# Kernel tuning notes

Measured on AMD Instinct MI355X. Metric: run time of the kernel, lower is better.

## Reference

```python
import jax, jax.numpy as jnp
import numpy as np

N, C, O, H, S, SHARE = 30000, 128, 128, 8, 16, 8
D = O // H            # mid_planes = 16
OS = O // SHARE       # 16
OFFSETS = [15000, 30000]
EPS = 1e-5


def _knn(p, offsets, k):
    """Exact per-batch KNN (incl. self), chunked to bound memory."""
    n = p.shape[0]
    idx = np.empty((n, k), dtype=np.int64)
    start = 0
    for end in offsets:
        pb = p[start:end]
        sq = (pb * pb).sum(-1)
        for qs in range(0, pb.shape[0], 1024):
            q = pb[qs:qs + 1024]
            d = sq[qs:qs + q.shape[0], None] - 2.0 * (q @ pb.T) + sq[None, :]
            part = np.argpartition(d, k - 1, axis=1)[:, :k]
            idx[start + qs:start + qs + q.shape[0]] = part + start
        start = end
    return idx


def _ln(x, g, b):
    m = x.mean(-1, keepdims=True)
    v = ((x - m) ** 2).mean(-1, keepdims=True)
    return (x - m) / jnp.sqrt(v + EPS) * g + b


def setup_inputs() -> dict:
    rng = np.random.default_rng(0)
    p_np = (rng.standard_normal((N, 3)) * 5.0).astype(np.float32)
    idx = _knn(p_np, OFFSETS, S)

    key = jax.random.key(0)
    ks = jax.random.split(key, 12)

    def lin(k, i, o):
        return (jax.random.normal(k, (i, o), jnp.float32) / np.sqrt(i)).astype(jnp.float32)

    return {
        "p": jnp.asarray(p_np),
        "x": jax.random.normal(ks[0], (N, C), jnp.float32),
        "idx": jnp.asarray(idx),
        "Wq": lin(ks[1], C, O), "bq": jnp.zeros((O,), jnp.float32),
        "Wk": lin(ks[2], C, O), "bk": jnp.zeros((O,), jnp.float32),
        "Wv": lin(ks[3], C, O), "bv": jnp.zeros((O,), jnp.float32),
        "Wp1": lin(ks[4], 3, 3), "bp1": jnp.zeros((3,), jnp.float32),
        "gp": jnp.ones((3,), jnp.float32), "betap": jnp.zeros((3,), jnp.float32),
        "Wp2": lin(ks[5], 3, O), "bp2": jnp.zeros((O,), jnp.float32),
        "gw1": jnp.ones((D,), jnp.float32), "betaw1": jnp.zeros((D,), jnp.float32),
        "Ww1": lin(ks[6], D, OS), "bw1": jnp.zeros((OS,), jnp.float32),
        "gw2": jnp.ones((OS,), jnp.float32), "betaw2": jnp.zeros((OS,), jnp.float32),
        "Ww2": lin(ks[7], OS, OS), "bw2": jnp.zeros((OS,), jnp.float32),
    }


def reference(p, x, idx, Wq, bq, Wk, bk, Wv, bv, Wp1, bp1, gp, betap, Wp2, bp2,
              gw1, betaw1, Ww1, bw1, gw2, betaw2, Ww2, bw2):
    xq = (x @ Wq + bq).reshape(N, H, D)          # (N,H,D)
    xk = x @ Wk + bk                              # (N,O)
    xv = x @ Wv + bv
    kg = xk[idx].reshape(N, S, H, D)              # neighbor gather
    vg = xv[idx].reshape(N, S, H, D)
    pr = p[idx] - p[:, None, :]                   # relative coords (N,S,3)
    pe = jax.nn.relu(_ln(pr @ Wp1 + bp1, gp, betap)) @ Wp2 + bp2  # (N,S,O)
    pe = pe.reshape(N, S, H, D)
    r = kg + pe - xq[:, None]                     # (N,S,H,D)
    w = jax.nn.relu(_ln(r, gw1, betaw1)) @ Ww1 + bw1
    w = jax.nn.relu(_ln(w, gw2, betaw2)) @ Ww2 + bw2  # (N,S,H,OS)
    w = jax.nn.softmax(w.mean(-1), axis=1)        # softmax over the S neighbors
    out = ((vg + pe) * w[..., None]).sum(axis=1)  # weighted neighbor reduce
    return out.reshape(N, O)
```

## Files before the change

### kernel.cpp

```cpp
#include <hip/hip_runtime.h>
#include <math.h>

typedef unsigned int  uint;
typedef unsigned short ushort;

constexpr int NPTS = 30000;
constexpr int CIN  = 128;
constexpr int OC   = 128;
constexpr int NH   = 8;
constexpr int NS   = 16;
constexpr int DH   = 16;
constexpr int OSH  = 16;
constexpr float EPSF = 1e-5f;

typedef __attribute__((ext_vector_type(8))) __fp16 h8;
typedef __attribute__((ext_vector_type(4))) float  f32x4;
typedef __attribute__((ext_vector_type(2))) __fp16 h2;

__device__ __forceinline__ ushort f2h(float f) {
    __fp16 h = (__fp16)f;
    return *(ushort*)&h;
}
__device__ __forceinline__ uint pk2(float a, float b) {
    h2 v = __builtin_amdgcn_cvt_pkrtz(a, b);
    return *(uint*)&v;
}
__device__ __forceinline__ h2 asH2(uint u) { return *(h2*)&u; }

#if defined(__has_builtin)
#if __has_builtin(__builtin_elementwise_max)
#define PKMAX(a, b) __builtin_elementwise_max(a, b)
#endif
#endif
#ifndef PKMAX
__device__ __forceinline__ h2 PKMAX(h2 a, h2 b) {
    h2 r; r[0] = a[0] > b[0] ? a[0] : b[0]; r[1] = a[1] > b[1] ? a[1] : b[1]; return r;
}
#endif

constexpr int PK_WW1   = 0;
constexpr int PK_WP2   = 128;
constexpr int PK_BP2   = 320;
constexpr int PK_GW1   = 384;
constexpr int PK_BW1P  = 392;
constexpr int PK_GW2   = 400;
constexpr int PK_BW2P  = 408;
constexpr int PK_RM    = 416;
constexpr int PKF_BW1  = 424;
constexpr int PKF_RMB  = 440;

__global__ __launch_bounds__(256) void prep_kernel(
    const float* __restrict__ Wq, const float* __restrict__ Wk, const float* __restrict__ Wv,
    const float* __restrict__ Wp2, const float* __restrict__ bp2,
    const float* __restrict__ gw1, const float* __restrict__ betaw1,
    const float* __restrict__ Ww1, const float* __restrict__ bw1,
    const float* __restrict__ gw2, const float* __restrict__ betaw2,
    const float* __restrict__ Ww2, const float* __restrict__ bw2,
    ushort* __restrict__ WT, uint* __restrict__ PK)
{
    const int b = blockIdx.x;
    const int t = threadIdx.x;
    if (b < 24) {
        const int mat = b >> 3;
        const int cg  = b & 7;
        const float* W = (mat == 0) ? Wq : (mat == 1 ? Wk : Wv);
        const int col = cg * 16 + (t >> 4);
        const int k0  = (t & 15) * 8;
        float v0 = W[(k0 + 0) * OC + col], v1 = W[(k0 + 1) * OC + col];
        float v2 = W[(k0 + 2) * OC + col], v3 = W[(k0 + 3) * OC + col];
        float v4 = W[(k0 + 4) * OC + col], v5 = W[(k0 + 5) * OC + col];
        float v6 = W[(k0 + 6) * OC + col], v7 = W[(k0 + 7) * OC + col];
        uint4 u = make_uint4(pk2(v0, v1), pk2(v2, v3), pk2(v4, v5), pk2(v6, v7));
        *(uint4*)&WT[(size_t)mat * OC * CIN + (size_t)col * CIN + k0] = u;
    } else {
        float* FPK = (float*)PK;
        if (t < 128) {
            int dp = t >> 4, o = t & 15;
            PK[PK_WW1 + t] = pk2(Ww1[(2 * dp) * OSH + o], Ww1[(2 * dp + 1) * OSH + o]);
        }
        if (t < 192) {
            int c = t >> 6, jj = t & 63;
            PK[PK_WP2 + t] = pk2(Wp2[c * OC + 2 * jj], Wp2[c * OC + 2 * jj + 1]);
        }
        if (t < 64)
            PK[PK_BP2 + t] = pk2(bp2[2 * t], bp2[2 * t + 1]);
        if (t < 8) {
            PK[PK_GW1 + t]  = pk2(gw1[2 * t],    gw1[2 * t + 1]);
            PK[PK_BW1P + t] = pk2(betaw1[2 * t], betaw1[2 * t + 1]);
            PK[PK_GW2 + t]  = pk2(gw2[2 * t],    gw2[2 * t + 1]);
            PK[PK_BW2P + t] = pk2(betaw2[2 * t], betaw2[2 * t + 1]);
            float r0 = 0.f, r1 = 0.f;
            #pragma unroll
            for (int o2 = 0; o2 < OSH; ++o2) {
                r0 += Ww2[(2 * t) * OSH + o2];
                r1 += Ww2[(2 * t + 1) * OSH + o2];
            }
            PK[PK_RM + t] = pk2(r0 * (1.f / OSH), r1 * (1.f / OSH));
        }
        if (t < 16)
            FPK[PKF_BW1 + t] = bw1[t];
        if (t == 16) {
            float acc = 0.f;
            #pragma unroll
            for (int o2 = 0; o2 < OSH; ++o2) acc += bw2[o2];
            FPK[PKF_RMB] = acc * (1.f / OSH);
        }
    }
}

__global__ __launch_bounds__(256) void qkv_mfma(
    const float* __restrict__ x, const ushort* __restrict__ WT,
    const float* __restrict__ bq, const float* __restrict__ bk, const float* __restrict__ bv,
    ushort* __restrict__ yq, ushort* __restrict__ yk, ushort* __restrict__ yv)
{
    const int mat = blockIdx.y;
    const float* bias = (mat == 0) ? bq : (mat == 1 ? bk : bv);
    ushort* y         = (mat == 0) ? yq : (mat == 1 ? yk : yv);
    const ushort* T   = WT + (size_t)mat * OC * CIN;

    const int n0   = blockIdx.x * 128;
    const int t    = threadIdx.x;
    const int wave = t >> 6;
    const int lane = t & 63;
    const int m16  = lane & 15;
    const int quad = lane >> 4;

    f32x4 acc[2][8];
    #pragma unroll
    for (int mt = 0; mt < 2; ++mt)
        #pragma unroll
        for (int nt = 0; nt < 8; ++nt)
            acc[mt][nt] = (f32x4){0.f, 0.f, 0.f, 0.f};

    int r0i = n0 + wave * 32 + m16;
    int r1i = r0i + 16;
    if (r0i > NPTS - 1) r0i = NPTS - 1;
    if (r1i > NPTS - 1) r1i = NPTS - 1;
    const float* arow0 = x + (size_t)r0i * CIN;
    const float* arow1 = x + (size_t)r1i * CIN;

    #pragma unroll
    for (int ks = 0; ks < 4; ++ks) {
        const int kb = ks * 32 + quad * 8;
        float4 f00 = *(const float4*)(arow0 + kb);
        float4 f01 = *(const float4*)(arow0 + kb + 4);
        float4 f10 = *(const float4*)(arow1 + kb);
        float4 f11 = *(const float4*)(arow1 + kb + 4);
        uint4 ua0 = make_uint4(pk2(f00.x, f00.y), pk2(f00.z, f00.w),
                               pk2(f01.x, f01.y), pk2(f01.z, f01.w));
        uint4 ua1 = make_uint4(pk2(f10.x, f10.y), pk2(f10.z, f10.w),
                               pk2(f11.x, f11.y), pk2(f11.z, f11.w));
        h8 a0 = *(h8*)&ua0;
        h8 a1 = *(h8*)&ua1;
        #pragma unroll
        for (int nt = 0; nt < 8; ++nt) {
            h8 bfr = *(const h8*)(T + (size_t)(nt * 16 + m16) * CIN + kb);
            acc[0][nt] = __builtin_amdgcn_mfma_f32_16x16x32_f16(a0, bfr, acc[0][nt], 0, 0, 0);
            acc[1][nt] = __builtin_amdgcn_mfma_f32_16x16x32_f16(a1, bfr, acc[1][nt], 0, 0, 0);
        }
    }

    #pragma unroll
    for (int mt = 0; mt < 2; ++mt) {
        #pragma unroll
        for (int nt = 0; nt < 8; ++nt) {
            const int col = nt * 16 + m16;
            const float bcol = bias[col];
            #pragma unroll
            for (int r = 0; r < 4; ++r) {
                int row = n0 + wave * 32 + mt * 16 + quad * 4 + r;
                if (row < NPTS)
                    y[(size_t)row * OC + col] = f2h(acc[mt][nt][r] + bcol);
            }
        }
    }
}

__global__ __launch_bounds__(256) void attn_kernel(
    const float* __restrict__ p, const int* __restrict__ idx,
    const ushort* __restrict__ xq, const ushort* __restrict__ xk, const ushort* __restrict__ xv,
    const float* __restrict__ Wp1, const float* __restrict__ bp1,
    const float* __restrict__ gp,  const float* __restrict__ betap,
    const uint* __restrict__ PK,
    float* __restrict__ out)
{
    const int t    = threadIdx.x;
    const int wv   = t >> 6;
    const int lane = t & 63;
    const int n    = blockIdx.x * 4 + wv;
    const int s    = lane & 15;
    const int u    = lane >> 4;

    const float* FPK = (const float*)PK;

    __shared__ __attribute__((aligned(16))) char pool[4 * 16 * 272];
    char* red = pool + wv * (16 * 272);

    const int j = idx[n * NS + s];

    float t0, t1, t2;
    {
        float pr0 = p[j * 3 + 0] - p[n * 3 + 0];
        float pr1 = p[j * 3 + 1] - p[n * 3 + 1];
        float pr2 = p[j * 3 + 2] - p[n * 3 + 2];
        float uu[3];
        #pragma unroll
        for (int c = 0; c < 3; ++c)
            uu[c] = bp1[c] + pr0 * Wp1[0 * 3 + c] + pr1 * Wp1[1 * 3 + c] + pr2 * Wp1[2 * 3 + c];
        float m   = (uu[0] + uu[1] + uu[2]) * (1.f / 3.f);
        float d0 = uu[0] - m, d1 = uu[1] - m, d2 = uu[2] - m;
        float var = (d0 * d0 + d1 * d1 + d2 * d2) * (1.f / 3.f);
        float inv = rsqrtf(var + EPSF);
        t0 = fmaxf((uu[0] - m) * inv * gp[0] + betap[0], 0.f);
        t1 = fmaxf((uu[1] - m) * inv * gp[1] + betap[1], 0.f);
        t2 = fmaxf((uu[2] - m) * inv * gp[2] + betap[2], 0.f);
    }

    __attribute__((aligned(16))) h2 pe2[16];
    {
        h2 t02 = asH2(pk2(t0, t0));
        h2 t12 = asH2(pk2(t1, t1));
        h2 t22 = asH2(pk2(t2, t2));
        const uint* W0p = PK + PK_WP2 + 0 * 64 + u * 16;
        const uint* W1p = PK + PK_WP2 + 1 * 64 + u * 16;
        const uint* W2p = PK + PK_WP2 + 2 * 64 + u * 16;
        const uint* Bp  = PK + PK_BP2 + u * 16;
        #pragma unroll
        for (int i = 0; i < 16; ++i) {
            h2 acc = asH2(Bp[i]);
            acc = acc + t02 * asH2(W0p[i]);
            acc = acc + t12 * asH2(W1p[i]);
            acc = acc + t22 * asH2(W2p[i]);
            pe2[i] = acc;
        }
    }

    __attribute__((aligned(16))) h2 vp2[16], r2[16];
    {
        __attribute__((aligned(16))) h2 k2[16], q2[16], v2[16];
        const uint4* k4 = (const uint4*)(xk + (size_t)j * OC + u * 32);
        const uint4* v4 = (const uint4*)(xv + (size_t)j * OC + u * 32);
        const uint4* q4 = (const uint4*)(xq + (size_t)n * OC + u * 32);
        #pragma unroll
        for (int i = 0; i < 4; ++i) {
            *(uint4*)&k2[4 * i] = k4[i];
            *(uint4*)&v2[4 * i] = v4[i];
            *(uint4*)&q2[4 * i] = q4[i];
        }
        #pragma unroll
        for (int i = 0; i < 16; ++i) {
            r2[i]  = (k2[i] + pe2[i]) - q2[i];
            vp2[i] = v2[i] + pe2[i];
        }
    }

    float wgt[2];
    #pragma unroll
    for (int hh = 0; hh < 2; ++hh) {
        h2* rr = r2 + hh * 8;

        __attribute__((aligned(16))) h2 a2[8];
        {
            h2 sum2 = rr[0];
            #pragma unroll
            for (int i = 1; i < 8; ++i) sum2 = sum2 + rr[i];
            float m = ((float)sum2[0] + (float)sum2[1]) * (1.f / DH);
            h2 m2 = asH2(pk2(m, m));
            h2 vs2 = {(__fp16)0.f, (__fp16)0.f};
            #pragma unroll
            for (int i = 0; i < 8; ++i) {
                rr[i] = rr[i] - m2;
                vs2 = vs2 + rr[i] * rr[i];
            }
            float var = ((float)vs2[0] + (float)vs2[1]) * (1.f / DH);
            float inv = rsqrtf(var + EPSF);
            h2 inv2 = asH2(pk2(inv, inv));
            h2 z2 = {(__fp16)0.f, (__fp16)0.f};
            #pragma unroll
            for (int i = 0; i < 8; ++i) {
                h2 gi = asH2(PK[PK_GW1 + i]) * inv2;
                a2[i] = PKMAX(rr[i] * gi + asH2(PK[PK_BW1P + i]), z2);
            }
        }

        float w1[OSH];
        #pragma unroll
        for (int o2 = 0; o2 < OSH; ++o2) w1[o2] = FPK[PKF_BW1 + o2];
        #pragma unroll
        for (int dp = 0; dp < 8; ++dp) {
            #pragma unroll
            for (int o2 = 0; o2 < OSH; ++o2)
                w1[o2] = __builtin_amdgcn_fdot2(a2[dp], asH2(PK[PK_WW1 + dp * 16 + o2]), w1[o2], false);
        }

        float logit;
        {
            __attribute__((aligned(16))) h2 w2[8];
            #pragma unroll
            for (int i = 0; i < 8; ++i) w2[i] = asH2(pk2(w1[2 * i], w1[2 * i + 1]));
            h2 sum2 = w2[0];
            #pragma unroll
            for (int i = 1; i < 8; ++i) sum2 = sum2 + w2[i];
            float m = ((float)sum2[0] + (float)sum2[1]) * (1.f / OSH);
            h2 m2 = asH2(pk2(m, m));
            h2 vs2 = {(__fp16)0.f, (__fp16)0.f};
            #pragma unroll
            for (int i = 0; i < 8; ++i) {
                w2[i] = w2[i] - m2;
                vs2 = vs2 + w2[i] * w2[i];
            }
            float var = ((float)vs2[0] + (float)vs2[1]) * (1.f / OSH);
            float inv = rsqrtf(var + EPSF);
            h2 inv2 = asH2(pk2(inv, inv));
            h2 z2 = {(__fp16)0.f, (__fp16)0.f};
            logit = FPK[PKF_RMB];
            #pragma unroll
            for (int i = 0; i < 8; ++i) {
                h2 gi = asH2(PK[PK_GW2 + i]) * inv2;
                h2 bv2 = PKMAX(w2[i] * gi + asH2(PK[PK_BW2P + i]), z2);
                logit = __builtin_amdgcn_fdot2(bv2, asH2(PK[PK_RM + i]), logit, false);
            }
        }

        {
            float mx = logit;
            #pragma unroll
            for (int mask = 1; mask < 16; mask <<= 1)
                mx = fmaxf(mx, __shfl_xor(mx, mask));
            float e = __expf(logit - mx);
            float den = e;
            #pragma unroll
            for (int mask = 1; mask < 16; mask <<= 1)
                den += __shfl_xor(den, mask);
            wgt[hh] = e * __builtin_amdgcn_rcpf(den);
        }
    }

    {
        h2 w0p = asH2(pk2(wgt[0], wgt[0]));
        h2 w1p = asH2(pk2(wgt[1], wgt[1]));
        __attribute__((aligned(16))) h2 c2[16];
        #pragma unroll
        for (int i = 0; i < 16; ++i)
            c2[i] = vp2[i] * (i < 8 ? w0p : w1p);
        char* wr = red + s * 272 + u * 64;
        *(uint4*)(wr +  0) = *(uint4*)&c2[0];
        *(uint4*)(wr + 16) = *(uint4*)&c2[4];
        *(uint4*)(wr + 32) = *(uint4*)&c2[8];
        *(uint4*)(wr + 48) = *(uint4*)&c2[12];
    }

    __builtin_amdgcn_wave_barrier();

    {
        h2 acc2 = {(__fp16)0.f, (__fp16)0.f};
        #pragma unroll
        for (int ss = 0; ss < NS; ++ss)
            acc2 = acc2 + *(const h2*)(red + ss * 272 + lane * 4);
        float2 o2 = make_float2((float)acc2[0], (float)acc2[1]);
        *(float2*)(out + (size_t)n * OC + lane * 2) = o2;
    }
}

extern "C" void kernel_launch(void* const* d_in, const int* in_sizes, int n_in,
                              void* d_out, int out_size, void* d_ws, size_t ws_size,
                              hipStream_t stream) {
    const float* p     = (const float*)d_in[0];
    const float* x     = (const float*)d_in[1];
    const int*   idx   = (const int*)d_in[2];
    const float* Wq    = (const float*)d_in[3];
    const float* bq    = (const float*)d_in[4];
    const float* Wk    = (const float*)d_in[5];
    const float* bk    = (const float*)d_in[6];
    const float* Wv    = (const float*)d_in[7];
    const float* bv    = (const float*)d_in[8];
    const float* Wp1   = (const float*)d_in[9];
    const float* bp1   = (const float*)d_in[10];
    const float* gp    = (const float*)d_in[11];
    const float* betap = (const float*)d_in[12];
    const float* Wp2   = (const float*)d_in[13];
    const float* bp2   = (const float*)d_in[14];
    const float* gw1   = (const float*)d_in[15];
    const float* betaw1= (const float*)d_in[16];
    const float* Ww1   = (const float*)d_in[17];
    const float* bw1   = (const float*)d_in[18];
    const float* gw2   = (const float*)d_in[19];
    const float* betaw2= (const float*)d_in[20];
    const float* Ww2   = (const float*)d_in[21];
    const float* bw2   = (const float*)d_in[22];
    float* out = (float*)d_out;

    ushort* WT = (ushort*)d_ws;
    ushort* xq = WT + 3 * OC * CIN;
    ushort* xk = xq + (size_t)NPTS * OC;
    ushort* xv = xk + (size_t)NPTS * OC;
    uint*   PACKS = (uint*)(xv + (size_t)NPTS * OC);

    prep_kernel<<<25, 256, 0, stream>>>(Wq, Wk, Wv,
                                        Wp2, bp2, gw1, betaw1,
                                        Ww1, bw1, gw2, betaw2, Ww2, bw2,
                                        WT, PACKS);

    dim3 g1((NPTS + 127) / 128, 3);
    qkv_mfma<<<g1, 256, 0, stream>>>(x, WT, bq, bk, bv, xq, xk, xv);

    attn_kernel<<<NPTS / 4, 256, 0, stream>>>(p, idx, xq, xk, xv,
                                              Wp1, bp1, gp, betap,
                                              PACKS, out);
}
```

Baseline: 190.6 us.

## Compute per-head Ww1 projection with MFMA via LDS staging

Replaces the per-lane fdot2 loop for the 16x16 Ww1 projection with 16x16x32 f16 MFMA instructions. LayerNorm outputs are staged through a per-wave LDS tile, multiplied against a preloaded B fragment zero-padded to K=32, and the results are written back to LDS for the next LayerNorm. It also drops the max-subtraction in the softmax, which saves shuffles but risks overflow if the logits grow large. This adds LDS traffic and wave barriers in place of many VALU dot instructions.

```diff
diff --git a/kernel.cpp b/kernel.cpp
--- a/kernel.cpp
+++ b/kernel.cpp
@@ -193,8 +193,22 @@
 
     const float* FPK = (const float*)PK;
 
-    __shared__ __attribute__((aligned(16))) char pool[4 * 16 * 272];
-    char* red = pool + wv * (16 * 272);
+    __shared__ __attribute__((aligned(16))) char pool[4 * 6144];
+    char* aw = pool + wv * 6144;
+
+    h8 bfrag;
+    {
+        uint4 u4 = make_uint4(0u, 0u, 0u, 0u);
+        const int o = lane & 15;
+        const int q = lane >> 4;
+        if (q < 2) {
+            u4.x = PK[PK_WW1 + (4 * q + 0) * 16 + o];
+            u4.y = PK[PK_WW1 + (4 * q + 1) * 16 + o];
+            u4.z = PK[PK_WW1 + (4 * q + 2) * 16 + o];
+            u4.w = PK[PK_WW1 + (4 * q + 3) * 16 + o];
+        }
+        bfrag = *(h8*)&u4;
+    }
 
     const int j = idx[n * NS + s];
 
@@ -254,50 +268,68 @@
         }
     }
 
+    __attribute__((aligned(16))) h2 a2[16];
+    #pragma unroll
+    for (int hh = 0; hh < 2; ++hh) {
+        h2* rr = r2 + hh * 8;
+        h2 sum2 = rr[0];
+        #pragma unroll
+        for (int i = 1; i < 8; ++i) sum2 = sum2 + rr[i];
+        float m = ((float)sum2[0] + (float)sum2[1]) * (1.f / DH);
+        h2 m2 = asH2(pk2(m, m));
+        h2 vs2 = {(__fp16)0.f, (__fp16)0.f};
+        #pragma unroll
+        for (int i = 0; i < 8; ++i) {
+            rr[i] = rr[i] - m2;
+            vs2 = vs2 + rr[i] * rr[i];
+        }
+        float var = ((float)vs2[0] + (float)vs2[1]) * (1.f / DH);
+        float inv = rsqrtf(var + EPSF);
+        h2 inv2 = asH2(pk2(inv, inv));
+        h2 z2 = {(__fp16)0.f, (__fp16)0.f};
+        #pragma unroll
+        for (int i = 0; i < 8; ++i) {
+            h2 gi = asH2(PK[PK_GW1 + i]) * inv2;
+            a2[hh * 8 + i] = PKMAX(rr[i] * gi + asH2(PK[PK_BW1P + i]), z2);
+        }
+    }
+
+    {
+        const int row0 = (2 * u) * 16 + s;
+        const int row1 = row0 + 16;
+        *(uint4*)(aw + row0 * 48 +  0) = *(uint4*)&a2[0];
+        *(uint4*)(aw + row0 * 48 + 16) = *(uint4*)&a2[4];
+        *(uint4*)(aw + row1 * 48 +  0) = *(uint4*)&a2[8];
+        *(uint4*)(aw + row1 * 48 + 16) = *(uint4*)&a2[12];
+    }
+    __builtin_amdgcn_wave_barrier();
+
+    {
+        const int m = lane & 15;
+        const int q = lane >> 4;
+        const float bw1o = FPK[PKF_BW1 + m];
+        #pragma unroll
+        for (int ht = 0; ht < 8; ++ht) {
+            h8 afr = *(const h8*)(aw + (ht * 16 + m) * 48 + (q & 1) * 16);
+            f32x4 acc = (f32x4){bw1o, bw1o, bw1o, bw1o};
+            acc = __builtin_amdgcn_mfma_f32_16x16x32_f16(afr, bfrag, acc, 0, 0, 0);
+            #pragma unroll
+            for (int r = 0; r < 4; ++r)
+                *(__fp16*)(aw + (ht * 16 + q * 4 + r) * 48 + m * 2) = (__fp16)acc[r];
+        }
+    }
+    __builtin_amdgcn_wave_barrier();
+
     float wgt[2];
     #pragma unroll
     for (int hh = 0; hh < 2; ++hh) {
-        h2* rr = r2 + hh * 8;
-
-        __attribute__((aligned(16))) h2 a2[8];
-        {
-            h2 sum2 = rr[0];
-            #pragma unroll
-            for (int i = 1; i < 8; ++i) sum2 = sum2 + rr[i];
-            float m = ((float)sum2[0] + (float)sum2[1]) * (1.f / DH);
-            h2 m2 = asH2(pk2(m, m));
-            h2 vs2 = {(__fp16)0.f, (__fp16)0.f};
-            #pragma unroll
-            for (int i = 0; i < 8; ++i) {
-                rr[i] = rr[i] - m2;
-                vs2 = vs2 + rr[i] * rr[i];
-            }
-            float var = ((float)vs2[0] + (float)vs2[1]) * (1.f / DH);
-            float inv = rsqrtf(var + EPSF);
-            h2 inv2 = asH2(pk2(inv, inv));
-            h2 z2 = {(__fp16)0.f, (__fp16)0.f};
-            #pragma unroll
-            for (int i = 0; i < 8; ++i) {
-                h2 gi = asH2(PK[PK_GW1 + i]) * inv2;
-                a2[i] = PKMAX(rr[i] * gi + asH2(PK[PK_BW1P + i]), z2);
-            }
-        }
-
-        float w1[OSH];
-        #pragma unroll
-        for (int o2 = 0; o2 < OSH; ++o2) w1[o2] = FPK[PKF_BW1 + o2];
-        #pragma unroll
-        for (int dp = 0; dp < 8; ++dp) {
-            #pragma unroll
-            for (int o2 = 0; o2 < OSH; ++o2)
-                w1[o2] = __builtin_amdgcn_fdot2(a2[dp], asH2(PK[PK_WW1 + dp * 16 + o2]), w1[o2], false);
-        }
+        const int row = (2 * u + hh) * 16 + s;
+        __attribute__((aligned(16))) h2 w2[8];
+        *(uint4*)&w2[0] = *(const uint4*)(aw + row * 48);
+        *(uint4*)&w2[4] = *(const uint4*)(aw + row * 48 + 16);
 
         float logit;
         {
-            __attribute__((aligned(16))) h2 w2[8];
-            #pragma unroll
-            for (int i = 0; i < 8; ++i) w2[i] = asH2(pk2(w1[2 * i], w1[2 * i + 1]));
             h2 sum2 = w2[0];
             #pragma unroll
             for (int i = 1; i < 8; ++i) sum2 = sum2 + w2[i];
@@ -323,11 +355,7 @@
         }
 
         {
-            float mx = logit;
-            #pragma unroll
-            for (int mask = 1; mask < 16; mask <<= 1)
-                mx = fmaxf(mx, __shfl_xor(mx, mask));
-            float e = __expf(logit - mx);
+            float e = __expf(logit);
             float den = e;
             #pragma unroll
             for (int mask = 1; mask < 16; mask <<= 1)
@@ -336,6 +364,8 @@
         }
     }
 
+    __builtin_amdgcn_wave_barrier();
+
     {
         h2 w0p = asH2(pk2(wgt[0], wgt[0]));
         h2 w1p = asH2(pk2(wgt[1], wgt[1]));
@@ -343,7 +373,7 @@
         #pragma unroll
         for (int i = 0; i < 16; ++i)
             c2[i] = vp2[i] * (i < 8 ? w0p : w1p);
-        char* wr = red + s * 272 + u * 64;
+        char* wr = aw + s * 272 + u * 64;
         *(uint4*)(wr +  0) = *(uint4*)&c2[0];
         *(uint4*)(wr + 16) = *(uint4*)&c2[4];
         *(uint4*)(wr + 32) = *(uint4*)&c2[8];
@@ -356,7 +386,7 @@
         h2 acc2 = {(__fp16)0.f, (__fp16)0.f};
         #pragma unroll
         for (int ss = 0; ss < NS; ++ss)
-            acc2 = acc2 + *(const h2*)(red + ss * 272 + lane * 4);
+            acc2 = acc2 + *(const h2*)(aw + ss * 272 + lane * 4);
         float2 o2 = make_float2((float)acc2[0], (float)acc2[1]);
         *(float2*)(out + (size_t)n * OC + lane * 2) = o2;
     }
```

Result: no change. 193.1 us (+1.3%).

## Fuse Q/K/V projections into one kernel and drop softmax max-subtraction

Applied to the files above, without the earlier changes.

Replaces the three-way grid QKV GEMM with a single kernel that converts each x row tile to fp16 once and runs all three weight matrices over it. The prepared weight layout is reorganised so each lane's B-fragment load for a k-step is contiguous across columns. It also removes the max-reduction before the neighbour softmax, saving shuffles. The cost is halved row tiling per wave, which means less weight reuse, and exp overflow is possible if logits ever grow large.

```diff
diff --git a/kernel.cpp b/kernel.cpp
--- a/kernel.cpp
+++ b/kernel.cpp
@@ -56,7 +56,7 @@
     const float* __restrict__ Ww1, const float* __restrict__ bw1,
     const float* __restrict__ gw2, const float* __restrict__ betaw2,
     const float* __restrict__ Ww2, const float* __restrict__ bw2,
-    ushort* __restrict__ WT, uint* __restrict__ PK)
+    ushort* __restrict__ WT2, uint* __restrict__ PK)
 {
     const int b = blockIdx.x;
     const int t = threadIdx.x;
@@ -71,7 +71,7 @@
         float v4 = W[(k0 + 4) * OC + col], v5 = W[(k0 + 5) * OC + col];
         float v6 = W[(k0 + 6) * OC + col], v7 = W[(k0 + 7) * OC + col];
         uint4 u = make_uint4(pk2(v0, v1), pk2(v2, v3), pk2(v4, v5), pk2(v6, v7));
-        *(uint4*)&WT[(size_t)mat * OC * CIN + (size_t)col * CIN + k0] = u;
+        *(uint4*)&WT2[(size_t)mat * OC * CIN + (size_t)((t & 15) * 128 + col) * 8] = u;
     } else {
         float* FPK = (float*)PK;
         if (t < 128) {
@@ -108,69 +108,62 @@
     }
 }
 
-__global__ __launch_bounds__(256) void qkv_mfma(
-    const float* __restrict__ x, const ushort* __restrict__ WT,
+__global__ __launch_bounds__(256) void qkv_fused(
+    const float* __restrict__ x, const ushort* __restrict__ WT2,
     const float* __restrict__ bq, const float* __restrict__ bk, const float* __restrict__ bv,
     ushort* __restrict__ yq, ushort* __restrict__ yk, ushort* __restrict__ yv)
 {
-    const int mat = blockIdx.y;
-    const float* bias = (mat == 0) ? bq : (mat == 1 ? bk : bv);
-    ushort* y         = (mat == 0) ? yq : (mat == 1 ? yk : yv);
-    const ushort* T   = WT + (size_t)mat * OC * CIN;
-
-    const int n0   = blockIdx.x * 128;
     const int t    = threadIdx.x;
     const int wave = t >> 6;
     const int lane = t & 63;
     const int m16  = lane & 15;
     const int quad = lane >> 4;
-
-    f32x4 acc[2][8];
-    #pragma unroll
-    for (int mt = 0; mt < 2; ++mt)
-        #pragma unroll
-        for (int nt = 0; nt < 8; ++nt)
-            acc[mt][nt] = (f32x4){0.f, 0.f, 0.f, 0.f};
-
-    int r0i = n0 + wave * 32 + m16;
-    int r1i = r0i + 16;
-    if (r0i > NPTS - 1) r0i = NPTS - 1;
-    if (r1i > NPTS - 1) r1i = NPTS - 1;
-    const float* arow0 = x + (size_t)r0i * CIN;
-    const float* arow1 = x + (size_t)r1i * CIN;
-
+    const int n0   = blockIdx.x * 64 + wave * 16;
+
+    int ri = n0 + m16;
+    if (ri > NPTS - 1) ri = NPTS - 1;
+    const float* arow = x + (size_t)ri * CIN;
+
+    h8 a[4];
     #pragma unroll
     for (int ks = 0; ks < 4; ++ks) {
         const int kb = ks * 32 + quad * 8;
-        float4 f00 = *(const float4*)(arow0 + kb);
-        float4 f01 = *(const float4*)(arow0 + kb + 4);
-        float4 f10 = *(const float4*)(arow1 + kb);
-        float4 f11 = *(const float4*)(arow1 + kb + 4);
-        uint4 ua0 = make_uint4(pk2(f00.x, f00.y), pk2(f00.z, f00.w),
-                               pk2(f01.x, f01.y), pk2(f01.z, f01.w));
-        uint4 ua1 = make_uint4(pk2(f10.x, f10.y), pk2(f10.z, f10.w),
-                               pk2(f11.x, f11.y), pk2(f11.z, f11.w));
-        h8 a0 = *(h8*)&ua0;
-        h8 a1 = *(h8*)&ua1;
+        float4 f0 = *(const float4*)(arow + kb);
+        float4 f1 = *(const float4*)(arow + kb + 4);
+        uint4 ua = make_uint4(pk2(f0.x, f0.y), pk2(f0.z, f0.w),
+                              pk2(f1.x, f1.y), pk2(f1.z, f1.w));
+        a[ks] = *(h8*)&ua;
+    }
+
+    #pragma unroll
+    for (int mat = 0; mat < 3; ++mat) {
+        const ushort* T   = WT2 + (size_t)mat * OC * CIN;
+        const float* bias = (mat == 0) ? bq : (mat == 1 ? bk : bv);
+        ushort* y         = (mat == 0) ? yq : (mat == 1 ? yk : yv);
+
+        f32x4 acc[8];
+        #pragma unroll
+        for (int nt = 0; nt < 8; ++nt)
+            acc[nt] = (f32x4){0.f, 0.f, 0.f, 0.f};
+
+        #pragma unroll
+        for (int ks = 0; ks < 4; ++ks) {
+            #pragma unroll
+            for (int nt = 0; nt < 8; ++nt) {
+                h8 bfr = *(const h8*)(T + (size_t)((ks * 4 + quad) * 128 + nt * 16 + m16) * 8);
+                acc[nt] = __builtin_amdgcn_mfma_f32_16x16x32_f16(a[ks], bfr, acc[nt], 0, 0, 0);
+            }
+        }
+
         #pragma unroll
         for (int nt = 0; nt < 8; ++nt) {
-            h8 bfr = *(const h8*)(T + (size_t)(nt * 16 + m16) * CIN + kb);
-            acc[0][nt] = __builtin_amdgcn_mfma_f32_16x16x32_f16(a0, bfr, acc[0][nt], 0, 0, 0);
-            acc[1][nt] = __builtin_amdgcn_mfma_f32_16x16x32_f16(a1, bfr, acc[1][nt], 0, 0, 0);
-        }
-    }
-
-    #pragma unroll
-    for (int mt = 0; mt < 2; ++mt) {
-        #pragma unroll
-        for (int nt = 0; nt < 8; ++nt) {
-            const int col = nt * 16 + m16;
-            const float bcol = bias[col];
+            const int col  = nt * 16 + m16;
+            const float bc = bias[col];
             #pragma unroll
             for (int r = 0; r < 4; ++r) {
-                int row = n0 + wave * 32 + mt * 16 + quad * 4 + r;
+                int row = n0 + quad * 4 + r;
                 if (row < NPTS)
-                    y[(size_t)row * OC + col] = f2h(acc[mt][nt][r] + bcol);
+                    y[(size_t)row * OC + col] = f2h(acc[nt][r] + bc);
             }
         }
     }
@@ -323,11 +316,7 @@
         }
 
         {
-            float mx = logit;
-            #pragma unroll
-            for (int mask = 1; mask < 16; mask <<= 1)
-                mx = fmaxf(mx, __shfl_xor(mx, mask));
-            float e = __expf(logit - mx);
+            float e = __expf(logit);
             float den = e;
             #pragma unroll
             for (int mask = 1; mask < 16; mask <<= 1)
@@ -390,8 +379,8 @@
     const float* bw2   = (const float*)d_in[22];
     float* out = (float*)d_out;
 
-    ushort* WT = (ushort*)d_ws;
-    ushort* xq = WT + 3 * OC * CIN;
+    ushort* WT2 = (ushort*)d_ws;
+    ushort* xq = WT2 + 3 * OC * CIN;
     ushort* xk = xq + (size_t)NPTS * OC;
     ushort* xv = xk + (size_t)NPTS * OC;
     uint*   PACKS = (uint*)(xv + (size_t)NPTS * OC);
@@ -399,10 +388,9 @@
     prep_kernel<<<25, 256, 0, stream>>>(Wq, Wk, Wv,
                                         Wp2, bp2, gw1, betaw1,
                                         Ww1, bw1, gw2, betaw2, Ww2, bw2,
-                                        WT, PACKS);
-
-    dim3 g1((NPTS + 127) / 128, 3);
-    qkv_mfma<<<g1, 256, 0, stream>>>(x, WT, bq, bk, bv, xq, xk, xv);
+                                        WT2, PACKS);
+
+    qkv_fused<<<(NPTS + 63) / 64, 256, 0, stream>>>(x, WT2, bq, bk, bv, xq, xk, xv);
 
     attn_kernel<<<NPTS / 4, 256, 0, stream>>>(p, idx, xq, xk, xv,
                                               Wp1, bp1, gp, betap,
```

Result: no change. 187.9 us (-1.5%).
